# Kernel tuning notes

Measured on AMD Instinct MI355X. Metric: run time of the kernel, lower is better.

The kernel has to match this reference:

```python
import jax, jax.numpy as jnp
import numpy as np

HEADS = 4
HID = 64
IN_DIM = 128
N_WIRES, N_TERM, N_ACT = 50, 20, 10
NEG_SLOPE = 0.2


def gat_conv(x, src, dst, ea, W, We, a_src, a_dst, a_edge, bias, concat):
    """PyG GATConv with edge features, add_self_loops=True, fill_value='mean'."""
    N = x.shape[0]
    H, F = a_src.shape
    # --- add self loops; self-loop edge_attr = mean of incoming edge_attr ---
    deg = jax.ops.segment_sum(jnp.ones((ea.shape[0],), x.dtype), dst, num_segments=N)
    loop_attr = jax.ops.segment_sum(ea, dst, num_segments=N) / jnp.maximum(deg, 1.0)[:, None]
    ar = jnp.arange(N)
    src = jnp.concatenate([src, ar])
    dst = jnp.concatenate([dst, ar])
    ea = jnp.concatenate([ea, loop_attr], axis=0)
    # --- linear transforms ---
    h = (x @ W).reshape(N, H, F)                      # [N,H,F]
    a_s = jnp.einsum('nhf,hf->nh', h, a_src)          # [N,H]
    a_d = jnp.einsum('nhf,hf->nh', h, a_dst)
    he = (ea @ We).reshape(-1, H, F)                  # [E2,H,F]
    a_e = jnp.einsum('ehf,hf->eh', he, a_edge)        # [E2,H]
    # --- attention logits + softmax over edges grouped by destination ---
    alpha = jax.nn.leaky_relu(a_s[src] + a_d[dst] + a_e, negative_slope=NEG_SLOPE)
    amax = jax.ops.segment_max(alpha, dst, num_segments=N)
    ex = jnp.exp(alpha - amax[dst])
    denom = jax.ops.segment_sum(ex, dst, num_segments=N)
    alpha = ex / (denom[dst] + 1e-16)                 # [E2,H]
    # --- message passing: gather src feats, weight, scatter-sum to dst ---
    out = jax.ops.segment_sum(h[src] * alpha[..., None], dst, num_segments=N)  # [N,H,F]
    out = out.reshape(N, H * F) if concat else out.mean(axis=1)
    return out + bias


def setup_inputs() -> dict:
    key = jax.random.key(0)
    ks = jax.random.split(key, 24)
    N, E = 20000, 320000
    x = jax.random.normal(ks[0], (N, IN_DIM), jnp.float32)
    edge_index = jax.random.randint(ks[1], (2, E), 0, N, dtype=jnp.int64)
    edge_attr = jax.random.normal(ks[2], (E, 2), jnp.float32)
    s = 0.1
    p = {
        'W1': jax.random.normal(ks[3], (IN_DIM, HEADS * HID)) * s,
        'We1': jax.random.normal(ks[4], (2, HEADS * HID)) * s,
        'as1': jax.random.normal(ks[5], (HEADS, HID)) * s,
        'ad1': jax.random.normal(ks[6], (HEADS, HID)) * s,
        'ae1': jax.random.normal(ks[7], (HEADS, HID)) * s,
        'b1': jnp.zeros((HEADS * HID,), jnp.float32),
        'W2': jax.random.normal(ks[8], (HEADS * HID, HEADS * HID)) * s,
        'We2': jax.random.normal(ks[9], (2, HEADS * HID)) * s,
        'as2': jax.random.normal(ks[10], (HEADS, HID)) * s,
        'ad2': jax.random.normal(ks[11], (HEADS, HID)) * s,
        'ae2': jax.random.normal(ks[12], (HEADS, HID)) * s,
        'b2': jnp.zeros((HID,), jnp.float32),
        'Ww': jax.random.normal(ks[13], (HID, N_WIRES)) * s,
        'bw': jnp.zeros((N_WIRES,), jnp.float32),
        'Wt': jax.random.normal(ks[14], (HID, N_TERM)) * s,
        'bt': jnp.zeros((N_TERM,), jnp.float32),
        'Wa': jax.random.normal(ks[15], (HID, N_ACT)) * s,
        'ba': jnp.zeros((N_ACT,), jnp.float32),
    }
    return {'x': x, 'edge_index': edge_index, 'edge_attr': edge_attr, **p}


def reference(x, edge_index, edge_attr, W1, We1, as1, ad1, ae1, b1,
              W2, We2, as2, ad2, ae2, b2, Ww, bw, Wt, bt, Wa, ba):
    src, dst = edge_index[0], edge_index[1]
    h = jax.nn.elu(gat_conv(x, src, dst, edge_attr, W1, We1, as1, ad1, ae1, b1, True))
    h = jax.nn.elu(gat_conv(h, src, dst, edge_attr, W2, We2, as2, ad2, ae2, b2, False))
    wire_logits = h @ Ww + bw
    terminal_logits = h @ Wt + bt
    action_logits = h @ Wa + ba
    return (wire_logits, terminal_logits, action_logits)
```

## Files before the change

### kernel.cpp

```cpp
#include <hip/hip_runtime.h>
#include <math.h>

#define N_NODES 20000
#define N_EDGES 320000
#define D1      256
#define SCAP    64
#define NGEMM1  314
#define NSCAT   1250
#define NPREP   496

typedef __attribute__((ext_vector_type(8))) short    bf16x8;
typedef __attribute__((ext_vector_type(4))) float    f32x4;
typedef __attribute__((ext_vector_type(8))) unsigned short u16x8;

__device__ inline float wred_sum(float v) {
#pragma unroll
  for (int o = 32; o > 0; o >>= 1) v += __shfl_xor(v, o, 64);
  return v;
}

__device__ inline unsigned short f2b(float v) {
  unsigned u = __float_as_uint(v);
  unsigned r = (u + 0x7fffu + ((u >> 16) & 1u)) >> 16;
  return (unsigned short)r;
}
__device__ inline float b2f(unsigned short h) {
  return __uint_as_float(((unsigned)h) << 16);
}

__global__ __launch_bounds__(256) void k_prep(
    int* __restrict__ deg,
    const float* __restrict__ W1, unsigned short* __restrict__ WT1h,
    unsigned short* __restrict__ WT1l,
    const float* __restrict__ W2, unsigned short* __restrict__ WT2h,
    unsigned short* __restrict__ WT2l,
    const float* __restrict__ We1, const float* __restrict__ ae1,
    const float* __restrict__ We2, const float* __restrict__ ae2,
    float* __restrict__ qb,
    const float* __restrict__ Ww, const float* __restrict__ Wt,
    const float* __restrict__ Wa,
    const float* __restrict__ bw, const float* __restrict__ bt,
    const float* __restrict__ ba,
    unsigned short* __restrict__ WallTh, unsigned short* __restrict__ WallTl,
    float* __restrict__ biasAll) {
  int bid = blockIdx.x, t = threadIdx.x;
  if (bid < 128) {
    int i = bid * 256 + t;
    int k = i >> 8, n = i & 255;
    float v = W1[i];
    unsigned short h = f2b(v);
    WT1h[n * 128 + k] = h;
    WT1l[n * 128 + k] = f2b(v - b2f(h));
  } else if (bid < 384) {
    int i = (bid - 128) * 256 + t;
    int k = i >> 8, n = i & 255;
    float v = W2[i];
    unsigned short h = f2b(v);
    WT2h[n * 256 + k] = h;
    WT2l[n * 256 + k] = f2b(v - b2f(h));
  } else if (bid == 384) {
    int lane = t & 63, w = t >> 6;
    const float* We = (w >> 1) ? We2 : We1;
    const float* ae = (w >> 1) ? ae2 : ae1;
    int c = w & 1;
#pragma unroll
    for (int h = 0; h < 4; h++) {
      float p = We[c * D1 + h * 64 + lane] * ae[h * 64 + lane];
      p = wred_sum(p);
      if (lane == 0) qb[(w >> 1) * 8 + c * 4 + h] = p;
    }
    if (t < 80) biasAll[t] = (t < 50) ? bw[t] : (t < 70) ? bt[t - 50] : ba[t - 70];
  } else if (bid < 417) {
    int i = (bid - 385) * 256 + t;
    int j = i >> 6, f = i & 63;
    float v = 0.f;
    if (j < 50)      v = Ww[f * 50 + j];
    else if (j < 70) v = Wt[f * 20 + (j - 50)];
    else if (j < 80) v = Wa[f * 10 + (j - 70)];
    unsigned short h = f2b(v);
    WallTh[j * 64 + f] = h;
    WallTl[j * 64 + f] = f2b(v - b2f(h));
  } else {
    int i = (bid - 417) * 256 + t;
    if (i < N_NODES) deg[i] = 0;
  }
}

#define LDK 40

__global__ __launch_bounds__(256) void k_fused1(
    const float* __restrict__ Af,
    const unsigned short* __restrict__ BTh, const unsigned short* __restrict__ BTl,
    unsigned short* __restrict__ Chi,
    const float* __restrict__ asw, const float* __restrict__ adw,
    float* __restrict__ asb, float* __restrict__ adb, int M,
    const int* __restrict__ ei, const float* __restrict__ ea,
    int* __restrict__ deg, int4* __restrict__ slot) {
  __shared__ unsigned short sAh[128 * LDK];
  __shared__ unsigned short sBh[128 * LDK], sBl[128 * LDK];
  const int K = 128;
  int bid = blockIdx.x, tid = threadIdx.x;

  if (bid >= NGEMM1) {
    int e = (bid - NGEMM1) * 256 + tid;
    int s = ei[e], d = ei[N_EDGES + e];
    float2 e2 = *(const float2*)&ea[e * 2];
    int pos = atomicAdd(&deg[d], 1);
    if (pos < SCAP) {
      int4 rec;
      rec.x = s; rec.y = __float_as_int(e2.x);
      rec.z = __float_as_int(e2.y); rec.w = 0;
      slot[(size_t)d * SCAP + pos] = rec;
    }
    return;
  }

  int lane = tid & 63, wid = tid >> 6;
  int wr = wid >> 1, wc = wid & 1;
  int row0 = (bid >> 1) * 128, col0 = (bid & 1) * 128;
  int aRow = wr * 64, bRow = wc * 64;

  f32x4 acc[4][4];
#pragma unroll
  for (int i = 0; i < 4; i++)
#pragma unroll
    for (int j = 0; j < 4; j++) acc[i][j] = (f32x4){0.f, 0.f, 0.f, 0.f};

  int c0i = tid * 2;
  int r0 = c0i >> 2, ko0 = (c0i & 3) * 8;
  int c1i = tid * 2 + 1;
  int r1 = c1i >> 2, ko1 = (c1i & 3) * 8;
  int q8 = (lane >> 4) * 8;
  int rsel = lane & 15;

  const u16x8 z8 = {0, 0, 0, 0, 0, 0, 0, 0};
  int ga0 = row0 + r0, ga1 = row0 + r1;
  bool va0 = ga0 < M, va1 = ga1 < M;
  size_t arow0 = (size_t)ga0 * K, arow1 = (size_t)ga1 * K;
  size_t brow0 = (size_t)(col0 + r0) * K, brow1 = (size_t)(col0 + r1) * K;

  auto ldA = [&](size_t rowoff, bool valid, int kk) -> u16x8 {
    if (!valid) return z8;
    float4 f0 = *(const float4*)&Af[rowoff + kk];
    float4 f1 = *(const float4*)&Af[rowoff + kk + 4];
    u16x8 r;
    r[0] = f2b(f0.x); r[1] = f2b(f0.y); r[2] = f2b(f0.z); r[3] = f2b(f0.w);
    r[4] = f2b(f1.x); r[5] = f2b(f1.y); r[6] = f2b(f1.z); r[7] = f2b(f1.w);
    return r;
  };

  u16x8 ca0 = ldA(arow0, va0, ko0), ca1 = ldA(arow1, va1, ko1);
  u16x8 cbh0 = *(const u16x8*)&BTh[brow0 + ko0];
  u16x8 cbl0 = *(const u16x8*)&BTl[brow0 + ko0];
  u16x8 cbh1 = *(const u16x8*)&BTh[brow1 + ko1];
  u16x8 cbl1 = *(const u16x8*)&BTl[brow1 + ko1];

  for (int k0 = 0; k0 < K; k0 += 32) {
    *(u16x8*)&sAh[r0 * LDK + ko0] = ca0;
    *(u16x8*)&sAh[r1 * LDK + ko1] = ca1;
    *(u16x8*)&sBh[r0 * LDK + ko0] = cbh0;
    *(u16x8*)&sBl[r0 * LDK + ko0] = cbl0;
    *(u16x8*)&sBh[r1 * LDK + ko1] = cbh1;
    *(u16x8*)&sBl[r1 * LDK + ko1] = cbl1;
    __syncthreads();

    if (k0 + 32 < K) {
      int kn = k0 + 32;
      ca0 = ldA(arow0, va0, kn + ko0);
      ca1 = ldA(arow1, va1, kn + ko1);
      cbh0 = *(const u16x8*)&BTh[brow0 + kn + ko0];
      cbl0 = *(const u16x8*)&BTl[brow0 + kn + ko0];
      cbh1 = *(const u16x8*)&BTh[brow1 + kn + ko1];
      cbl1 = *(const u16x8*)&BTl[brow1 + kn + ko1];
    }

    bf16x8 fah[4], fbh[4], fbl[4];
#pragma unroll
    for (int i = 0; i < 4; i++) {
      int ar = aRow + i * 16 + rsel;
      int br = bRow + i * 16 + rsel;
      fah[i] = *(const bf16x8*)&sAh[ar * LDK + q8];
      fbh[i] = *(const bf16x8*)&sBh[br * LDK + q8];
      fbl[i] = *(const bf16x8*)&sBl[br * LDK + q8];
    }
#pragma unroll
    for (int i = 0; i < 4; i++)
#pragma unroll
      for (int j = 0; j < 4; j++) {
        acc[i][j] = __builtin_amdgcn_mfma_f32_16x16x32_bf16(fah[i], fbh[j], acc[i][j], 0, 0, 0);
        acc[i][j] = __builtin_amdgcn_mfma_f32_16x16x32_bf16(fah[i], fbl[j], acc[i][j], 0, 0, 0);
      }
    __syncthreads();
  }

  int rq = (lane >> 4) * 4;
  int head = (col0 + bRow) >> 6;
  float sa[4], sd[4];
#pragma unroll
  for (int j = 0; j < 4; j++) {
    sa[j] = asw[head * 64 + j * 16 + rsel];
    sd[j] = adw[head * 64 + j * 16 + rsel];
  }
#pragma unroll
  for (int i = 0; i < 4; i++) {
#pragma unroll
    for (int j = 0; j < 4; j++) {
      int gcol = col0 + bRow + j * 16 + rsel;
#pragma unroll
      for (int r = 0; r < 4; r++) {
        int grow = row0 + aRow + i * 16 + rq + r;
        if (grow < M) Chi[(size_t)grow * D1 + gcol] = f2b(acc[i][j][r]);
      }
    }
#pragma unroll
    for (int r = 0; r < 4; r++) {
      float ps = 0.f, pd = 0.f;
#pragma unroll
      for (int j = 0; j < 4; j++) {
        ps = fmaf(acc[i][j][r], sa[j], ps);
        pd = fmaf(acc[i][j][r], sd[j], pd);
      }
#pragma unroll
      for (int o = 1; o < 16; o <<= 1) {
        ps += __shfl_xor(ps, o, 64);
        pd += __shfl_xor(pd, o, 64);
      }
      int grow = row0 + aRow + i * 16 + rq + r;
      if ((lane & 15) == 0 && grow < M) {
        asb[grow * 4 + head] = ps;
        adb[grow * 4 + head] = pd;
      }
    }
  }
}

__global__ __launch_bounds__(256) void k_gemm_mfma(
    const unsigned short* __restrict__ Ah,
    const unsigned short* __restrict__ BTh, const unsigned short* __restrict__ BTl,
    unsigned short* __restrict__ Chi,
    const float* __restrict__ asw, const float* __restrict__ adw,
    float* __restrict__ asb, float* __restrict__ adb,
    int M, int K) {
  __shared__ unsigned short sAh[128 * LDK];
  __shared__ unsigned short sBh[128 * LDK], sBl[128 * LDK];
  int tid = threadIdx.x;
  int lane = tid & 63, wid = tid >> 6;
  int wr = wid >> 1, wc = wid & 1;
  int row0 = blockIdx.y * 128, col0 = blockIdx.x * 128;
  int aRow = wr * 64, bRow = wc * 64;

  f32x4 acc[4][4];
#pragma unroll
  for (int i = 0; i < 4; i++)
#pragma unroll
    for (int j = 0; j < 4; j++) acc[i][j] = (f32x4){0.f, 0.f, 0.f, 0.f};

  int c0i = tid * 2;
  int r0 = c0i >> 2, ko0 = (c0i & 3) * 8;
  int c1i = tid * 2 + 1;
  int r1 = c1i >> 2, ko1 = (c1i & 3) * 8;
  int q8 = (lane >> 4) * 8;
  int rsel = lane & 15;

  const u16x8 z8 = {0, 0, 0, 0, 0, 0, 0, 0};
  int ga0 = row0 + r0, ga1 = row0 + r1;
  bool va0 = ga0 < M, va1 = ga1 < M;
  size_t arow0 = (size_t)ga0 * K, arow1 = (size_t)ga1 * K;
  size_t brow0 = (size_t)(col0 + r0) * K, brow1 = (size_t)(col0 + r1) * K;

  u16x8 ca0 = va0 ? *(const u16x8*)&Ah[arow0 + ko0] : z8;
  u16x8 ca1 = va1 ? *(const u16x8*)&Ah[arow1 + ko1] : z8;
  u16x8 cbh0 = *(const u16x8*)&BTh[brow0 + ko0];
  u16x8 cbl0 = *(const u16x8*)&BTl[brow0 + ko0];
  u16x8 cbh1 = *(const u16x8*)&BTh[brow1 + ko1];
  u16x8 cbl1 = *(const u16x8*)&BTl[brow1 + ko1];

  for (int k0 = 0; k0 < K; k0 += 32) {
    *(u16x8*)&sAh[r0 * LDK + ko0] = ca0;
    *(u16x8*)&sAh[r1 * LDK + ko1] = ca1;
    *(u16x8*)&sBh[r0 * LDK + ko0] = cbh0;
    *(u16x8*)&sBl[r0 * LDK + ko0] = cbl0;
    *(u16x8*)&sBh[r1 * LDK + ko1] = cbh1;
    *(u16x8*)&sBl[r1 * LDK + ko1] = cbl1;
    __syncthreads();

    if (k0 + 32 < K) {
      int kn = k0 + 32;
      ca0 = va0 ? *(const u16x8*)&Ah[arow0 + kn + ko0] : z8;
      ca1 = va1 ? *(const u16x8*)&Ah[arow1 + kn + ko1] : z8;
      cbh0 = *(const u16x8*)&BTh[brow0 + kn + ko0];
      cbl0 = *(const u16x8*)&BTl[brow0 + kn + ko0];
      cbh1 = *(const u16x8*)&BTh[brow1 + kn + ko1];
      cbl1 = *(const u16x8*)&BTl[brow1 + kn + ko1];
    }

    bf16x8 fah[4], fbh[4], fbl[4];
#pragma unroll
    for (int i = 0; i < 4; i++) {
      int ar = aRow + i * 16 + rsel;
      int br = bRow + i * 16 + rsel;
      fah[i] = *(const bf16x8*)&sAh[ar * LDK + q8];
      fbh[i] = *(const bf16x8*)&sBh[br * LDK + q8];
      fbl[i] = *(const bf16x8*)&sBl[br * LDK + q8];
    }
#pragma unroll
    for (int i = 0; i < 4; i++)
#pragma unroll
      for (int j = 0; j < 4; j++) {
        acc[i][j] = __builtin_amdgcn_mfma_f32_16x16x32_bf16(fah[i], fbh[j], acc[i][j], 0, 0, 0);
        acc[i][j] = __builtin_amdgcn_mfma_f32_16x16x32_bf16(fah[i], fbl[j], acc[i][j], 0, 0, 0);
      }
    __syncthreads();
  }

  int rq = (lane >> 4) * 4;
  int head = (col0 + bRow) >> 6;
  float sa[4], sd[4];
#pragma unroll
  for (int j = 0; j < 4; j++) {
    sa[j] = asw[head * 64 + j * 16 + rsel];
    sd[j] = adw[head * 64 + j * 16 + rsel];
  }
#pragma unroll
  for (int i = 0; i < 4; i++) {
#pragma unroll
    for (int j = 0; j < 4; j++) {
      int gcol = col0 + bRow + j * 16 + rsel;
#pragma unroll
      for (int r = 0; r < 4; r++) {
        int grow = row0 + aRow + i * 16 + rq + r;
        if (grow < M) Chi[(size_t)grow * D1 + gcol] = f2b(acc[i][j][r]);
      }
    }
#pragma unroll
    for (int r = 0; r < 4; r++) {
      float ps = 0.f, pd = 0.f;
#pragma unroll
      for (int j = 0; j < 4; j++) {
        ps = fmaf(acc[i][j][r], sa[j], ps);
        pd = fmaf(acc[i][j][r], sd[j], pd);
      }
#pragma unroll
      for (int o = 1; o < 16; o <<= 1) {
        ps += __shfl_xor(ps, o, 64);
        pd += __shfl_xor(pd, o, 64);
      }
      int grow = row0 + aRow + i * 16 + rq + r;
      if ((lane & 15) == 0 && grow < M) {
        asb[grow * 4 + head] = ps;
        adb[grow * 4 + head] = pd;
      }
    }
  }
}

__global__ __launch_bounds__(256) void k_heads_mfma(
    const unsigned short* __restrict__ Ah, const unsigned short* __restrict__ Al,
    const unsigned short* __restrict__ BTh, const unsigned short* __restrict__ BTl,
    const float* __restrict__ biasAll, float* __restrict__ out, int M) {
  __shared__ unsigned short sAh[128 * LDK], sAl[128 * LDK];
  __shared__ unsigned short sBh[128 * LDK], sBl[128 * LDK];
  const int K = 64;
  int tid = threadIdx.x;
  int lane = tid & 63, wid = tid >> 6;
  int wr = wid >> 1, wc = wid & 1;
  int row0 = blockIdx.x * 128;
  int aRow = wr * 64, bRow = wc * 64;

  f32x4 acc[4][4];
#pragma unroll
  for (int i = 0; i < 4; i++)
#pragma unroll
    for (int j = 0; j < 4; j++) acc[i][j] = (f32x4){0.f, 0.f, 0.f, 0.f};

  int c0i = tid * 2;
  int r0 = c0i >> 2, ko0 = (c0i & 3) * 8;
  int c1i = tid * 2 + 1;
  int r1 = c1i >> 2, ko1 = (c1i & 3) * 8;
  int q8 = (lane >> 4) * 8;
  int rsel = lane & 15;

  for (int k0 = 0; k0 < K; k0 += 32) {
    u16x8 z = {0, 0, 0, 0, 0, 0, 0, 0};
    int ga0 = row0 + r0, ga1 = row0 + r1;
    u16x8 vah0 = (ga0 < M) ? *(const u16x8*)&Ah[(size_t)ga0 * K + k0 + ko0] : z;
    u16x8 val0 = (ga0 < M) ? *(const u16x8*)&Al[(size_t)ga0 * K + k0 + ko0] : z;
    u16x8 vah1 = (ga1 < M) ? *(const u16x8*)&Ah[(size_t)ga1 * K + k0 + ko1] : z;
    u16x8 val1 = (ga1 < M) ? *(const u16x8*)&Al[(size_t)ga1 * K + k0 + ko1] : z;
    u16x8 vbh0 = *(const u16x8*)&BTh[(size_t)r0 * K + k0 + ko0];
    u16x8 vbl0 = *(const u16x8*)&BTl[(size_t)r0 * K + k0 + ko0];
    u16x8 vbh1 = *(const u16x8*)&BTh[(size_t)r1 * K + k0 + ko1];
    u16x8 vbl1 = *(const u16x8*)&BTl[(size_t)r1 * K + k0 + ko1];
    *(u16x8*)&sAh[r0 * LDK + ko0] = vah0;
    *(u16x8*)&sAl[r0 * LDK + ko0] = val0;
    *(u16x8*)&sAh[r1 * LDK + ko1] = vah1;
    *(u16x8*)&sAl[r1 * LDK + ko1] = val1;
    *(u16x8*)&sBh[r0 * LDK + ko0] = vbh0;
    *(u16x8*)&sBl[r0 * LDK + ko0] = vbl0;
    *(u16x8*)&sBh[r1 * LDK + ko1] = vbh1;
    *(u16x8*)&sBl[r1 * LDK + ko1] = vbl1;
    __syncthreads();

    bf16x8 fah[4], fal[4], fbh[4], fbl[4];
#pragma unroll
    for (int i = 0; i < 4; i++) {
      int ar = aRow + i * 16 + rsel;
      int br = bRow + i * 16 + rsel;
      fah[i] = *(const bf16x8*)&sAh[ar * LDK + q8];
      fal[i] = *(const bf16x8*)&sAl[ar * LDK + q8];
      fbh[i] = *(const bf16x8*)&sBh[br * LDK + q8];
      fbl[i] = *(const bf16x8*)&sBl[br * LDK + q8];
    }
#pragma unroll
    for (int i = 0; i < 4; i++)
#pragma unroll
      for (int j = 0; j < 4; j++) {
        acc[i][j] = __builtin_amdgcn_mfma_f32_16x16x32_bf16(fah[i], fbh[j], acc[i][j], 0, 0, 0);
        acc[i][j] = __builtin_amdgcn_mfma_f32_16x16x32_bf16(fah[i], fbl[j], acc[i][j], 0, 0, 0);
        acc[i][j] = __builtin_amdgcn_mfma_f32_16x16x32_bf16(fal[i], fbh[j], acc[i][j], 0, 0, 0);
      }
    __syncthreads();
  }

  int rq = (lane >> 4) * 4;
#pragma unroll
  for (int j = 0; j < 4; j++) {
    int gcol = bRow + j * 16 + rsel;
    if (gcol < 80) {
      float bj = biasAll[gcol];
      float* op; int cols, jj;
      if (gcol < 50)      { op = out;                 cols = 50; jj = gcol; }
      else if (gcol < 70) { op = out + N_NODES * 50;  cols = 20; jj = gcol - 50; }
      else                { op = out + N_NODES * 70;  cols = 10; jj = gcol - 70; }
#pragma unroll
      for (int i = 0; i < 4; i++) {
#pragma unroll
        for (int r = 0; r < 4; r++) {
          int grow = row0 + aRow + i * 16 + rq + r;
          if (grow < M) op[(size_t)grow * cols + jj] = acc[i][j][r] + bj;
        }
      }
    }
  }
}

template <bool CONCAT>
__global__ __launch_bounds__(256) void k_aggregate(
    const unsigned short* __restrict__ feath,
    const int* __restrict__ deg_arr, const int4* __restrict__ slot,
    const float* __restrict__ asb, const float* __restrict__ adb,
    const float* __restrict__ q, const float* __restrict__ bias,
    unsigned short* __restrict__ outh,
    unsigned short* __restrict__ outf_h, unsigned short* __restrict__ outf_l) {
  __shared__ float slog[4][SCAP][4];
  __shared__ int   ssrc[4][SCAP];
  int t = threadIdx.x, lane = t & 63, w = t >> 6;
  int n = blockIdx.x * 4 + w;
  int deg = min(deg_arr[n], SCAP);

  float4 qv0 = *(const float4*)q;
  float4 qv1 = *(const float4*)(q + 4);
  float4 ad4 = *(const float4*)&adb[(size_t)n * 4];
  float4 asn = *(const float4*)&asb[(size_t)n * 4];

  int degR = (deg + 15) & ~15;
  if (degR == 0) degR = 16;
  int   sreg = n;
  float e0v = 0.f, e1v = 0.f;
  if (lane < degR) {
    if (lane < deg) {
      int4 rec = slot[(size_t)n * SCAP + lane];
      sreg = rec.x; e0v = __int_as_float(rec.y); e1v = __int_as_float(rec.z);
    }
    ssrc[w][lane] = sreg;
  }
  float l0 = -1e30f, l1 = -1e30f, l2 = -1e30f, l3 = -1e30f;
  if (lane < deg) {
    float4 as4 = *(const float4*)&asb[(size_t)sreg * 4];
    l0 = as4.x + ad4.x + e0v * qv0.x + e1v * qv1.x; l0 = (l0 > 0.f) ? l0 : 0.2f * l0;
    l1 = as4.y + ad4.y + e0v * qv0.y + e1v * qv1.y; l1 = (l1 > 0.f) ? l1 : 0.2f * l1;
    l2 = as4.z + ad4.z + e0v * qv0.z + e1v * qv1.z; l2 = (l2 > 0.f) ? l2 : 0.2f * l2;
    l3 = as4.w + ad4.w + e0v * qv0.w + e1v * qv1.w; l3 = (l3 > 0.f) ? l3 : 0.2f * l3;
  }
  float dinv = 1.f / fmaxf((float)deg, 1.f);
  float e0m = wred_sum(e0v) * dinv;
  float e1m = wred_sum(e1v) * dinv;
  float ls[4];
  ls[0] = asn.x + ad4.x + e0m * qv0.x + e1m * qv1.x;
  ls[1] = asn.y + ad4.y + e0m * qv0.y + e1m * qv1.y;
  ls[2] = asn.z + ad4.z + e0m * qv0.z + e1m * qv1.z;
  ls[3] = asn.w + ad4.w + e0m * qv0.w + e1m * qv1.w;
#pragma unroll
  for (int h = 0; h < 4; h++) ls[h] = (ls[h] > 0.f) ? ls[h] : 0.2f * ls[h];
  float ex[4] = {__expf(l0), __expf(l1), __expf(l2), __expf(l3)};
  float inv[4], wself[4];
#pragma unroll
  for (int h = 0; h < 4; h++) {
    float eself = __expf(ls[h]);
    float ss = wred_sum(ex[h]) + eself;
    inv[h] = 1.f / (ss + 1e-16f);
    wself[h] = eself * inv[h];
  }
  if (lane < degR) {
    *(f32x4*)&slog[w][lane][0] = (f32x4){ex[0] * inv[0], ex[1] * inv[1],
                                         ex[2] * inv[2], ex[3] * inv[3]};
  }
  int es = lane >> 5, cg = lane & 31, hh = cg >> 3;
  const unsigned short* fb = feath + cg * 8;
  float acc8[8] = {};
  for (int j0 = 0; j0 < degR; j0 += 16) {
    u16x8 f[8];
#pragma unroll
    for (int q8 = 0; q8 < 8; q8++)
      f[q8] = *(const u16x8*)&fb[(size_t)ssrc[w][j0 + 2 * q8 + es] * D1];
#pragma unroll
    for (int q8 = 0; q8 < 8; q8++) {
      float ww = slog[w][j0 + 2 * q8 + es][hh];
#pragma unroll
      for (int k = 0; k < 8; k++) acc8[k] = fmaf(ww, b2f((unsigned short)f[q8][k]), acc8[k]);
    }
  }
  if (es == 0) {
    u16x8 fs = *(const u16x8*)&fb[(size_t)n * D1];
    float ws2 = wself[hh];
#pragma unroll
    for (int k = 0; k < 8; k++) acc8[k] = fmaf(ws2, b2f((unsigned short)fs[k]), acc8[k]);
  }
#pragma unroll
  for (int k = 0; k < 8; k++) acc8[k] += __shfl_xor(acc8[k], 32, 64);
  if constexpr (CONCAT) {
    if (es == 0) {
      u16x8 hi8;
#pragma unroll
      for (int k = 0; k < 8; k++) {
        float v2 = acc8[k] + bias[cg * 8 + k];
        v2 = (v2 > 0.f) ? v2 : (__expf(v2) - 1.f);
        hi8[k] = f2b(v2);
      }
      *(u16x8*)&outh[(size_t)n * D1 + cg * 8] = hi8;
    }
  } else {
#pragma unroll
    for (int k = 0; k < 8; k++) {
      acc8[k] += __shfl_xor(acc8[k], 8, 64);
      acc8[k] += __shfl_xor(acc8[k], 16, 64);
    }
    if (es == 0 && cg < 8) {
      u16x8 hi8, lo8;
#pragma unroll
      for (int k = 0; k < 8; k++) {
        float v2 = acc8[k] * 0.25f + bias[cg * 8 + k];
        v2 = (v2 > 0.f) ? v2 : (__expf(v2) - 1.f);
        unsigned short hh2 = f2b(v2);
        hi8[k] = hh2;
        lo8[k] = f2b(v2 - b2f(hh2));
      }
      *(u16x8*)&outf_h[(size_t)n * 64 + cg * 8] = hi8;
      *(u16x8*)&outf_l[(size_t)n * 64 + cg * 8] = lo8;
    }
  }
}

extern "C" void kernel_launch(void* const* d_in, const int* in_sizes, int n_in,
                              void* d_out, int out_size, void* d_ws, size_t ws_size,
                              hipStream_t stream) {
  const float* x   = (const float*)d_in[0];
  const int*   ei  = (const int*)d_in[1];
  const float* ea  = (const float*)d_in[2];
  const float* W1  = (const float*)d_in[3];
  const float* We1 = (const float*)d_in[4];
  const float* as1 = (const float*)d_in[5];
  const float* ad1 = (const float*)d_in[6];
  const float* ae1 = (const float*)d_in[7];
  const float* b1  = (const float*)d_in[8];
  const float* W2  = (const float*)d_in[9];
  const float* We2 = (const float*)d_in[10];
  const float* as2 = (const float*)d_in[11];
  const float* ad2 = (const float*)d_in[12];
  const float* ae2 = (const float*)d_in[13];
  const float* b2  = (const float*)d_in[14];
  const float* Ww  = (const float*)d_in[15];
  const float* bw  = (const float*)d_in[16];
  const float* Wt  = (const float*)d_in[17];
  const float* bt  = (const float*)d_in[18];
  const float* Wa  = (const float*)d_in[19];
  const float* ba  = (const float*)d_in[20];
  float* out = (float*)d_out;

  char* ws = (char*)d_ws;
  size_t off = 0;
  auto alloc = [&](size_t bytes) {
    void* p = ws + off;
    off += (bytes + 255) & ~(size_t)255;
    return p;
  };
  unsigned short* Ah     = (unsigned short*)alloc((size_t)N_NODES * D1 * 2);
  unsigned short* Bfh    = (unsigned short*)alloc((size_t)N_NODES * D1 * 2);
  unsigned short* h2h    = (unsigned short*)alloc((size_t)N_NODES * 64 * 2);
  unsigned short* h2l    = (unsigned short*)alloc((size_t)N_NODES * 64 * 2);
  unsigned short* WT1h   = (unsigned short*)alloc((size_t)128 * 256 * 2);
  unsigned short* WT1l   = (unsigned short*)alloc((size_t)128 * 256 * 2);
  unsigned short* WT2h   = (unsigned short*)alloc((size_t)256 * 256 * 2);
  unsigned short* WT2l   = (unsigned short*)alloc((size_t)256 * 256 * 2);
  unsigned short* WallTh = (unsigned short*)alloc((size_t)128 * 64 * 2);
  unsigned short* WallTl = (unsigned short*)alloc((size_t)128 * 64 * 2);
  float*          biasAll= (float*)alloc(80 * 4);
  int4*  slot    = (int4*)alloc((size_t)N_NODES * SCAP * 16);
  int*   deg     = (int*)alloc((size_t)N_NODES * 4);
  float* asb     = (float*)alloc((size_t)N_NODES * 4 * 4);
  float* adb     = (float*)alloc((size_t)N_NODES * 4 * 4);
  float* qb      = (float*)alloc(64);

  k_prep<<<NPREP, 256, 0, stream>>>(
      deg, W1, WT1h, WT1l, W2, WT2h, WT2l, We1, ae1, We2, ae2, qb,
      Ww, Wt, Wa, bw, bt, ba, WallTh, WallTl, biasAll);

  k_fused1<<<NGEMM1 + NSCAT, 256, 0, stream>>>(
      x, WT1h, WT1l, Ah, as1, ad1, asb, adb, N_NODES, ei, ea, deg, slot);

  k_aggregate<true><<<N_NODES / 4, 256, 0, stream>>>(
      Ah, deg, slot, asb, adb, qb, b1, Bfh, nullptr, nullptr);

  dim3 ggemm(2, (N_NODES + 127) / 128);
  k_gemm_mfma<<<ggemm, 256, 0, stream>>>(Bfh, WT2h, WT2l, Ah,
                                         as2, ad2, asb, adb, N_NODES, 256);
  k_aggregate<false><<<N_NODES / 4, 256, 0, stream>>>(
      Ah, deg, slot, asb, adb, qb + 8, b2, nullptr, h2h, h2l);

  k_heads_mfma<<<(N_NODES + 127) / 128, 256, 0, stream>>>(
      h2h, h2l, WallTh, WallTl, biasAll, out, N_NODES);
}
```

Baseline: 218.0 us.

## Fuse output heads projection into second-layer aggregation epilogue

```diff
diff --git a/kernel.cpp b/kernel.cpp
--- a/kernel.cpp
+++ b/kernel.cpp
@@ -7,7 +7,7 @@
 #define SCAP    64
 #define NGEMM1  314
 #define NSCAT   1250
-#define NPREP   496
+#define NPREP   484
 
 typedef __attribute__((ext_vector_type(8))) short    bf16x8;
 typedef __attribute__((ext_vector_type(4))) float    f32x4;
@@ -38,11 +38,7 @@
     const float* __restrict__ We2, const float* __restrict__ ae2,
     float* __restrict__ qb,
     const float* __restrict__ Ww, const float* __restrict__ Wt,
-    const float* __restrict__ Wa,
-    const float* __restrict__ bw, const float* __restrict__ bt,
-    const float* __restrict__ ba,
-    unsigned short* __restrict__ WallTh, unsigned short* __restrict__ WallTl,
-    float* __restrict__ biasAll) {
+    const float* __restrict__ Wa, float* __restrict__ WallT) {
   int bid = blockIdx.x, t = threadIdx.x;
   if (bid < 128) {
     int i = bid * 256 + t;
@@ -69,19 +65,14 @@
       p = wred_sum(p);
       if (lane == 0) qb[(w >> 1) * 8 + c * 4 + h] = p;
     }
-    if (t < 80) biasAll[t] = (t < 50) ? bw[t] : (t < 70) ? bt[t - 50] : ba[t - 70];
-  } else if (bid < 417) {
+  } else if (bid < 405) {
     int i = (bid - 385) * 256 + t;
     int j = i >> 6, f = i & 63;
-    float v = 0.f;
-    if (j < 50)      v = Ww[f * 50 + j];
-    else if (j < 70) v = Wt[f * 20 + (j - 50)];
-    else if (j < 80) v = Wa[f * 10 + (j - 70)];
-    unsigned short h = f2b(v);
-    WallTh[j * 64 + f] = h;
-    WallTl[j * 64 + f] = f2b(v - b2f(h));
+    WallT[i] = (j < 50) ? Ww[f * 50 + j]
+             : (j < 70) ? Wt[f * 20 + (j - 50)]
+                        : Wa[f * 10 + (j - 70)];
   } else {
-    int i = (bid - 417) * 256 + t;
+    int i = (bid - 405) * 256 + t;
     if (i < N_NODES) deg[i] = 0;
   }
 }
@@ -354,96 +345,6 @@
   }
 }
 
-__global__ __launch_bounds__(256) void k_heads_mfma(
-    const unsigned short* __restrict__ Ah, const unsigned short* __restrict__ Al,
-    const unsigned short* __restrict__ BTh, const unsigned short* __restrict__ BTl,
-    const float* __restrict__ biasAll, float* __restrict__ out, int M) {
-  __shared__ unsigned short sAh[128 * LDK], sAl[128 * LDK];
-  __shared__ unsigned short sBh[128 * LDK], sBl[128 * LDK];
-  const int K = 64;
-  int tid = threadIdx.x;
-  int lane = tid & 63, wid = tid >> 6;
-  int wr = wid >> 1, wc = wid & 1;
-  int row0 = blockIdx.x * 128;
-  int aRow = wr * 64, bRow = wc * 64;
-
-  f32x4 acc[4][4];
-#pragma unroll
-  for (int i = 0; i < 4; i++)
-#pragma unroll
-    for (int j = 0; j < 4; j++) acc[i][j] = (f32x4){0.f, 0.f, 0.f, 0.f};
-
-  int c0i = tid * 2;
-  int r0 = c0i >> 2, ko0 = (c0i & 3) * 8;
-  int c1i = tid * 2 + 1;
-  int r1 = c1i >> 2, ko1 = (c1i & 3) * 8;
-  int q8 = (lane >> 4) * 8;
-  int rsel = lane & 15;
-
-  for (int k0 = 0; k0 < K; k0 += 32) {
-    u16x8 z = {0, 0, 0, 0, 0, 0, 0, 0};
-    int ga0 = row0 + r0, ga1 = row0 + r1;
-    u16x8 vah0 = (ga0 < M) ? *(const u16x8*)&Ah[(size_t)ga0 * K + k0 + ko0] : z;
-    u16x8 val0 = (ga0 < M) ? *(const u16x8*)&Al[(size_t)ga0 * K + k0 + ko0] : z;
-    u16x8 vah1 = (ga1 < M) ? *(const u16x8*)&Ah[(size_t)ga1 * K + k0 + ko1] : z;
-    u16x8 val1 = (ga1 < M) ? *(const u16x8*)&Al[(size_t)ga1 * K + k0 + ko1] : z;
-    u16x8 vbh0 = *(const u16x8*)&BTh[(size_t)r0 * K + k0 + ko0];
-    u16x8 vbl0 = *(const u16x8*)&BTl[(size_t)r0 * K + k0 + ko0];
-    u16x8 vbh1 = *(const u16x8*)&BTh[(size_t)r1 * K + k0 + ko1];
-    u16x8 vbl1 = *(const u16x8*)&BTl[(size_t)r1 * K + k0 + ko1];
-    *(u16x8*)&sAh[r0 * LDK + ko0] = vah0;
-    *(u16x8*)&sAl[r0 * LDK + ko0] = val0;
-    *(u16x8*)&sAh[r1 * LDK + ko1] = vah1;
-    *(u16x8*)&sAl[r1 * LDK + ko1] = val1;
-    *(u16x8*)&sBh[r0 * LDK + ko0] = vbh0;
-    *(u16x8*)&sBl[r0 * LDK + ko0] = vbl0;
-    *(u16x8*)&sBh[r1 * LDK + ko1] = vbh1;
-    *(u16x8*)&sBl[r1 * LDK + ko1] = vbl1;
-    __syncthreads();
-
-    bf16x8 fah[4], fal[4], fbh[4], fbl[4];
-#pragma unroll
-    for (int i = 0; i < 4; i++) {
-      int ar = aRow + i * 16 + rsel;
-      int br = bRow + i * 16 + rsel;
-      fah[i] = *(const bf16x8*)&sAh[ar * LDK + q8];
-      fal[i] = *(const bf16x8*)&sAl[ar * LDK + q8];
-      fbh[i] = *(const bf16x8*)&sBh[br * LDK + q8];
-      fbl[i] = *(const bf16x8*)&sBl[br * LDK + q8];
-    }
-#pragma unroll
-    for (int i = 0; i < 4; i++)
-#pragma unroll
-      for (int j = 0; j < 4; j++) {
-        acc[i][j] = __builtin_amdgcn_mfma_f32_16x16x32_bf16(fah[i], fbh[j], acc[i][j], 0, 0, 0);
-        acc[i][j] = __builtin_amdgcn_mfma_f32_16x16x32_bf16(fah[i], fbl[j], acc[i][j], 0, 0, 0);
-        acc[i][j] = __builtin_amdgcn_mfma_f32_16x16x32_bf16(fal[i], fbh[j], acc[i][j], 0, 0, 0);
-      }
-    __syncthreads();
-  }
-
-  int rq = (lane >> 4) * 4;
-#pragma unroll
-  for (int j = 0; j < 4; j++) {
-    int gcol = bRow + j * 16 + rsel;
-    if (gcol < 80) {
-      float bj = biasAll[gcol];
-      float* op; int cols, jj;
-      if (gcol < 50)      { op = out;                 cols = 50; jj = gcol; }
-      else if (gcol < 70) { op = out + N_NODES * 50;  cols = 20; jj = gcol - 50; }
-      else                { op = out + N_NODES * 70;  cols = 10; jj = gcol - 70; }
-#pragma unroll
-      for (int i = 0; i < 4; i++) {
-#pragma unroll
-        for (int r = 0; r < 4; r++) {
-          int grow = row0 + aRow + i * 16 + rq + r;
-          if (grow < M) op[(size_t)grow * cols + jj] = acc[i][j][r] + bj;
-        }
-      }
-    }
-  }
-}
-
 template <bool CONCAT>
 __global__ __launch_bounds__(256) void k_aggregate(
     const unsigned short* __restrict__ feath,
@@ -451,7 +352,9 @@
     const float* __restrict__ asb, const float* __restrict__ adb,
     const float* __restrict__ q, const float* __restrict__ bias,
     unsigned short* __restrict__ outh,
-    unsigned short* __restrict__ outf_h, unsigned short* __restrict__ outf_l) {
+    const float* __restrict__ WallT,
+    const float* __restrict__ bw, const float* __restrict__ bt,
+    const float* __restrict__ ba, float* __restrict__ out) {
   __shared__ float slog[4][SCAP][4];
   __shared__ int   ssrc[4][SCAP];
   int t = threadIdx.x, lane = t & 63, w = t >> 6;
@@ -540,23 +443,48 @@
       *(u16x8*)&outh[(size_t)n * D1 + cg * 8] = hi8;
     }
   } else {
+    __shared__ float sW[80 * 65];
+    __shared__ float sh2[4][64];
+    for (int i = t; i < 80 * 64; i += 256) {
+      int j = i >> 6, f = i & 63;
+      sW[j * 65 + f] = WallT[i];
+    }
 #pragma unroll
     for (int k = 0; k < 8; k++) {
       acc8[k] += __shfl_xor(acc8[k], 8, 64);
       acc8[k] += __shfl_xor(acc8[k], 16, 64);
     }
     if (es == 0 && cg < 8) {
-      u16x8 hi8, lo8;
+      float vv[8];
 #pragma unroll
       for (int k = 0; k < 8; k++) {
         float v2 = acc8[k] * 0.25f + bias[cg * 8 + k];
-        v2 = (v2 > 0.f) ? v2 : (__expf(v2) - 1.f);
-        unsigned short hh2 = f2b(v2);
-        hi8[k] = hh2;
-        lo8[k] = f2b(v2 - b2f(hh2));
-      }
-      *(u16x8*)&outf_h[(size_t)n * 64 + cg * 8] = hi8;
-      *(u16x8*)&outf_l[(size_t)n * 64 + cg * 8] = lo8;
+        vv[k] = (v2 > 0.f) ? v2 : (__expf(v2) - 1.f);
+      }
+      *(float4*)&sh2[w][cg * 8]     = (float4){vv[0], vv[1], vv[2], vv[3]};
+      *(float4*)&sh2[w][cg * 8 + 4] = (float4){vv[4], vv[5], vv[6], vv[7]};
+    }
+    __syncthreads();
+    const float* h2w = sh2[w];
+    {
+      int j = lane;
+      float a = 0.f;
+#pragma unroll
+      for (int f = 0; f < 64; f++) a = fmaf(h2w[f], sW[j * 65 + f], a);
+      float* op; int cols, jj; float bj;
+      if (j < 50)      { op = out;                cols = 50; jj = j;      bj = bw[j];      }
+      else             { op = out + N_NODES * 50; cols = 20; jj = j - 50; bj = bt[j - 50]; }
+      op[(size_t)n * cols + jj] = a + bj;
+    }
+    if (lane < 16) {
+      int j = 64 + lane;
+      float a = 0.f;
+#pragma unroll
+      for (int f = 0; f < 64; f++) a = fmaf(h2w[f], sW[j * 65 + f], a);
+      float* op; int cols, jj; float bj;
+      if (j < 70)      { op = out + N_NODES * 50; cols = 20; jj = j - 50; bj = bt[j - 50]; }
+      else             { op = out + N_NODES * 70; cols = 10; jj = j - 70; bj = ba[j - 70]; }
+      op[(size_t)n * cols + jj] = a + bj;
     }
   }
 }
@@ -596,15 +524,11 @@
   };
   unsigned short* Ah     = (unsigned short*)alloc((size_t)N_NODES * D1 * 2);
   unsigned short* Bfh    = (unsigned short*)alloc((size_t)N_NODES * D1 * 2);
-  unsigned short* h2h    = (unsigned short*)alloc((size_t)N_NODES * 64 * 2);
-  unsigned short* h2l    = (unsigned short*)alloc((size_t)N_NODES * 64 * 2);
   unsigned short* WT1h   = (unsigned short*)alloc((size_t)128 * 256 * 2);
   unsigned short* WT1l   = (unsigned short*)alloc((size_t)128 * 256 * 2);
   unsigned short* WT2h   = (unsigned short*)alloc((size_t)256 * 256 * 2);
   unsigned short* WT2l   = (unsigned short*)alloc((size_t)256 * 256 * 2);
-  unsigned short* WallTh = (unsigned short*)alloc((size_t)128 * 64 * 2);
-  unsigned short* WallTl = (unsigned short*)alloc((size_t)128 * 64 * 2);
-  float*          biasAll= (float*)alloc(80 * 4);
+  float* WallT   = (float*)alloc((size_t)80 * 64 * 4);
   int4*  slot    = (int4*)alloc((size_t)N_NODES * SCAP * 16);
   int*   deg     = (int*)alloc((size_t)N_NODES * 4);
   float* asb     = (float*)alloc((size_t)N_NODES * 4 * 4);
@@ -613,20 +537,19 @@
 
   k_prep<<<NPREP, 256, 0, stream>>>(
       deg, W1, WT1h, WT1l, W2, WT2h, WT2l, We1, ae1, We2, ae2, qb,
-      Ww, Wt, Wa, bw, bt, ba, WallTh, WallTl, biasAll);
+      Ww, Wt, Wa, WallT);
 
   k_fused1<<<NGEMM1 + NSCAT, 256, 0, stream>>>(
       x, WT1h, WT1l, Ah, as1, ad1, asb, adb, N_NODES, ei, ea, deg, slot);
 
   k_aggregate<true><<<N_NODES / 4, 256, 0, stream>>>(
-      Ah, deg, slot, asb, adb, qb, b1, Bfh, nullptr, nullptr);
+      Ah, deg, slot, asb, adb, qb, b1, Bfh,
+      nullptr, nullptr, nullptr, nullptr, nullptr);
 
   dim3 ggemm(2, (N_NODES + 127) / 128);
   k_gemm_mfma<<<ggemm, 256, 0, stream>>>(Bfh, WT2h, WT2l, Ah,
                                          as2, ad2, asb, adb, N_NODES, 256);
   k_aggregate<false><<<N_NODES / 4, 256, 0, stream>>>(
-      Ah, deg, slot, asb, adb, qb + 8, b2, nullptr, h2h, h2l);
-
-  k_heads_mfma<<<(N_NODES + 127) / 128, 256, 0, stream>>>(
-      h2h, h2l, WallTh, WallTl, biasAll, out, N_NODES);
-}
+      Ah, deg, slot, asb, adb, qb + 8, b2, nullptr,
+      WallT, bw, bt, ba, out);
+}
```

Result: slower. 231.4 us (+6.1%).
